# Kernel optimization log

Measured on AMD Instinct MI355X. Metric: run time of the kernel, lower is better.

The kernel has to match this reference:

```python
import jax, jax.numpy as jnp
import numpy as np

T, N, E = 64, 50000, 1600000
DYN, STAT, GH, RH = 1, 6, 32, 64


def setup_inputs() -> dict:
    key = jax.random.key(0)
    ks = jax.random.split(key, 12)
    s = 0.05
    return {
        "dyn_seq": jax.random.normal(ks[0], (T, N, DYN), jnp.float32),
        "static": jax.random.normal(ks[1], (N, STAT), jnp.float32),
        "edge_index": jax.random.randint(ks[2], (2, E), 0, N, jnp.int32),
        "gcn_w0": s * jax.random.normal(ks[3], (DYN + STAT, GH), jnp.float32),
        "gcn_b0": jnp.zeros((GH,), jnp.float32),
        "gcn_w1": s * jax.random.normal(ks[4], (GH, GH), jnp.float32),
        "gcn_b1": jnp.zeros((GH,), jnp.float32),
        "w_ih": s * jax.random.normal(ks[5], (3 * RH, GH), jnp.float32),
        "w_hh": s * jax.random.normal(ks[6], (3 * RH, RH), jnp.float32),
        "b_ih": jnp.zeros((3 * RH,), jnp.float32),
        "b_hh": jnp.zeros((3 * RH,), jnp.float32),
        "mlp_w1": s * jax.random.normal(ks[7], (RH, RH), jnp.float32),
        "mlp_b1": jnp.zeros((RH,), jnp.float32),
        "mlp_w2": s * jax.random.normal(ks[8], (1, RH), jnp.float32),
        "mlp_b2": jnp.zeros((1,), jnp.float32),
    }


def reference(dyn_seq, static, edge_index, gcn_w0, gcn_b0, gcn_w1, gcn_b1,
              w_ih, w_hh, b_ih, b_hh, mlp_w1, mlp_b1, mlp_w2, mlp_b2):
    n = static.shape[0]
    # GCNConv normalization (PyG default): add self-loops, sym norm D^-1/2 (A+I) D^-1/2
    loops = jnp.arange(n, dtype=edge_index.dtype)
    src = jnp.concatenate([edge_index[0], loops])
    dst = jnp.concatenate([edge_index[1], loops])
    deg = jax.ops.segment_sum(jnp.ones_like(dst, jnp.float32), dst, num_segments=n)
    dinv = jnp.where(deg > 0, jax.lax.rsqrt(deg), 0.0)
    norm = (dinv[src] * dinv[dst])[:, None]  # [E+N, 1]

    def gcn(h, w, b):
        h = h @ w  # transform first (small feature dim), then aggregate
        agg = jax.ops.segment_sum(h[src] * norm, dst, num_segments=n)
        return jax.nn.relu(agg + b)

    def step(x_t):  # x_t: [N, DYN]
        x = jnp.concatenate([x_t, static], axis=1)
        return gcn(gcn(x, gcn_w0, gcn_b0), gcn_w1, gcn_b1)

    H = jax.lax.map(step, dyn_seq)  # [T, N, GH] (sequential over T to bound memory)

    rh = w_hh.shape[1]

    def gru_step(h, x_t):  # torch nn.GRU cell math
        gx = x_t @ w_ih.T + b_ih
        gh = h @ w_hh.T + b_hh
        xr, xz, xn = jnp.split(gx, 3, axis=-1)
        hr, hz, hn = jnp.split(gh, 3, axis=-1)
        r = jax.nn.sigmoid(xr + hr)
        z = jax.nn.sigmoid(xz + hz)
        cand = jnp.tanh(xn + r * hn)
        h_new = (1.0 - z) * cand + z * h
        return h_new, None

    h0 = jnp.zeros((n, rh), H.dtype)
    h_last, _ = jax.lax.scan(gru_step, h0, H)  # last GRU output == out[:, -1, :]
    hid = jax.nn.relu(h_last @ mlp_w1.T + mlp_b1)
    return (hid @ mlp_w2.T + mlp_b2).squeeze(-1)  # [N]
```

## Files before the change

### kernel.cpp

```cpp
#include <hip/hip_runtime.h>
#include <hip/hip_bf16.h>

#define T_   64
#define N_   50000
#define E_   1600000
#define GH_  32
#define RH_  64
#define TB32_ 32
#define G32B_ 12500
#define GB_  782
#define NB_  196
#define AB_  12500

typedef _Float16 half_t;
typedef __attribute__((ext_vector_type(8))) _Float16 half8;
typedef __attribute__((ext_vector_type(4))) _Float16 half4;
typedef __attribute__((ext_vector_type(4))) float f32x4;
typedef __attribute__((ext_vector_type(4))) int i32x4;

static __device__ __forceinline__ float fast_sigmoid(float v) {
    float e = __expf(-v);
    return __builtin_amdgcn_rcpf(1.0f + e);
}
static __device__ __forceinline__ float fast_tanh(float v) {
    return 2.0f * fast_sigmoid(2.0f * v) - 1.0f;
}


__global__ __launch_bounds__(256)
void k_transpose(const float* __restrict__ dyn, half_t* __restrict__ dynT) {
    __shared__ float tile[64][65];
    int n0 = blockIdx.x * 64;
    int tx = threadIdx.x, ty = threadIdx.y;
#pragma unroll
    for (int r = 0; r < 16; ++r) {
        int t = r * 4 + ty;
        int n = n0 + tx;
        tile[t][tx] = (n < N_) ? dyn[(size_t)t * N_ + n] : 0.0f;
    }
    __syncthreads();
#pragma unroll
    for (int r = 0; r < 16; ++r) {
        int nl = r * 4 + ty;
        int n = n0 + nl;
        if (n < N_) dynT[(size_t)n * 64 + tx] = (half_t)tile[tx][nl];
    }
}

__global__ void k_hist(const int* __restrict__ src, const int* __restrict__ dst,
                       int* __restrict__ cnt) {
    int e = blockIdx.x * blockDim.x + threadIdx.x;
    if (e >= E_) return;
    atomicAdd(&cnt[dst[e] * 16 + (src[e] >> 12)], 1);
}

__global__ __launch_bounds__(256)
void k_scanA(const int* __restrict__ cnt, int* __restrict__ deg,
             int* __restrict__ row_ptr, int* __restrict__ bsum) {
    __shared__ int buf[256];
    int tid = threadIdx.x;
    int i = blockIdx.x * 256 + tid;
    int v = 0;
    if (i < N_) {
        const int4* c4 = (const int4*)(cnt + i * 16);
#pragma unroll
        for (int c = 0; c < 4; ++c) {
            int4 w = c4[c];
            v += w.x + w.y + w.z + w.w;
        }
        deg[i] = v;
    }
    buf[tid] = v;
    __syncthreads();
#pragma unroll
    for (int off = 1; off < 256; off <<= 1) {
        int t = (tid >= off) ? buf[tid - off] : 0;
        __syncthreads();
        buf[tid] += t;
        __syncthreads();
    }
    if (i < N_) row_ptr[i + 1] = buf[tid];
    if (tid == 255) bsum[blockIdx.x] = buf[255];
}
__global__ __launch_bounds__(256)
void k_scanB(int* __restrict__ bsum, int nb) {
    __shared__ int buf[256];
    int tid = threadIdx.x;
    buf[tid] = (tid < nb) ? bsum[tid] : 0;
    __syncthreads();
#pragma unroll
    for (int off = 1; off < 256; off <<= 1) {
        int t = (tid >= off) ? buf[tid - off] : 0;
        __syncthreads();
        buf[tid] += t;
        __syncthreads();
    }
    if (tid < nb) bsum[tid] = (tid > 0) ? buf[tid - 1] : 0;
}
__global__ __launch_bounds__(256)
void k_scanC(int* __restrict__ row_ptr, const int* __restrict__ bsum) {
    int i = blockIdx.x * 256 + threadIdx.x;
    if (i == 0) row_ptr[0] = 0;
    if (i < N_) row_ptr[i + 1] += bsum[blockIdx.x];
}

__global__ __launch_bounds__(256)
void k_rowscan(const int* __restrict__ row_ptr, int* __restrict__ cnt,
               int* __restrict__ rp2) {
    int n = blockIdx.x * 256 + threadIdx.x;
    if (n >= N_) return;
    int run = row_ptr[n];
#pragma unroll
    for (int t = 0; t < 16; ++t) {
        int c = cnt[n * 16 + t];
        rp2[n * 16 + t] = run;
        run += c;
        cnt[n * 16 + t] = 0;
    }
}

__global__ __launch_bounds__(256)
void k_node_init(const int* __restrict__ deg,
                 const float* __restrict__ statics,
                 const float* __restrict__ w0,
                 float* __restrict__ dinv,
                 float* __restrict__ selfn,
                 half_t* __restrict__ h0s) {
    int n = blockIdx.x * blockDim.x + threadIdx.x;
    if (n >= N_) return;
    float d  = (float)deg[n] + 1.0f;
    float di = rsqrtf(d);
    dinv[n] = di;
    selfn[n] = di * di;
    float s[6];
#pragma unroll
    for (int j = 0; j < 6; ++j) s[j] = statics[n * 6 + j];
    half8 o[4];
#pragma unroll
    for (int k = 0; k < GH_; ++k) {
        float v = 0.0f;
#pragma unroll
        for (int j = 0; j < 6; ++j) v += s[j] * w0[(1 + j) * GH_ + k];
        o[k >> 3][k & 7] = (half_t)v;
    }
    half8* dst8 = (half8*)(h0s + (size_t)n * GH_);
#pragma unroll
    for (int c = 0; c < 4; ++c) dst8[c] = o[c];
}

__global__ void k_scatter2(const int* __restrict__ src, const int* __restrict__ dst,
                           const float* __restrict__ dinv,
                           const int* __restrict__ rp2, int* __restrict__ cnt,
                           int2* __restrict__ erec) {
    int e = blockIdx.x * blockDim.x + threadIdx.x;
    if (e >= E_) return;
    int s = src[e], d = dst[e];
    int slot = d * 16 + (s >> 12);
    int pos = rp2[slot] + atomicAdd(&cnt[slot], 1);
    erec[pos] = make_int2(s, __float_as_int(dinv[s] * dinv[d]));
}

__global__ void k_wB(const float* __restrict__ wih, const float* __restrict__ whh,
                     half_t* __restrict__ wB) {
    int idx = blockIdx.x * 256 + threadIdx.x;
    if (idx >= 96 * 192) return;
    int j = idx & 7;
    int r = idx >> 3;
    int m = r & 15; r >>= 4;
    int q = r & 3;  r >>= 2;
    int nt = r % 12;
    int c = r / 12;
    int k = c * 32 + q * 8 + j;
    int col = nt * 16 + m;
    float v = (k < 32) ? wih[col * 32 + k] : whh[col * 64 + (k - 32)];
    wB[idx] = (half_t)v;
}

__global__ void k_w1B(const float* __restrict__ w1, half_t* __restrict__ w1B) {
    int idx = blockIdx.x * 256 + threadIdx.x;
    if (idx >= 1024) return;
    int j = idx & 7;
    int m = (idx >> 3) & 15;
    int q = (idx >> 7) & 3;
    int nt = idx >> 9;
    w1B[idx] = (half_t)w1[(q * 8 + j) * GH_ + nt * 16 + m];
}


static __device__ __forceinline__
void aall_body(int bid, const int* __restrict__ row_ptr, const int2* __restrict__ erec,
               const float* __restrict__ selfn, const half_t* __restrict__ dynT,
               half_t* __restrict__ aTh) {
    int wv = __builtin_amdgcn_readfirstlane(threadIdx.x >> 6);
    int n = bid * 4 + wv;
    int lane = threadIdx.x & 63;
    float acc = selfn[n] * (float)dynT[(size_t)n * 64 + lane];
    int e0 = row_ptr[n], e1 = row_ptr[n + 1];
    int e = e0;
    for (; e < e1 && (e & 3); ++e) {
        int2 r = erec[e];
        acc += __int_as_float(r.y) * (float)dynT[(size_t)r.x * 64 + lane];
    }
    for (; e + 4 <= e1; e += 4) {
        int4 p0 = *(const int4*)(erec + e);
        int4 p1 = *(const int4*)(erec + e + 2);
        float v0 = (float)dynT[(size_t)p0.x * 64 + lane];
        float v1 = (float)dynT[(size_t)p0.z * 64 + lane];
        float v2 = (float)dynT[(size_t)p1.x * 64 + lane];
        float v3 = (float)dynT[(size_t)p1.z * 64 + lane];
        acc += __int_as_float(p0.y) * v0 + __int_as_float(p0.w) * v1
             + __int_as_float(p1.y) * v2 + __int_as_float(p1.w) * v3;
    }
    for (; e < e1; ++e) {
        int2 r = erec[e];
        acc += __int_as_float(r.y) * (float)dynT[(size_t)r.x * 64 + lane];
    }
    aTh[(size_t)n * 64 + lane] = (half_t)acc;
}

static __device__ __forceinline__
void g16s_body(int bid, const int* __restrict__ row_ptr, const int2* __restrict__ erec,
               const float* __restrict__ selfn, const half_t* __restrict__ h0s,
               const float* __restrict__ b0, half_t* __restrict__ ch) {
    int gid = bid * 256 + threadIdx.x;
    int n = gid >> 2, q = gid & 3;
    if (n >= N_) return;
    const half8* f8 = (const half8*)h0s;
    float acc[8];
    {
        half8 sv = f8[(size_t)n * 4 + q];
        float sn = selfn[n];
#pragma unroll
        for (int i = 0; i < 8; ++i) acc[i] = sn * (float)sv[i];
    }
    int e0 = row_ptr[n], e1 = row_ptr[n + 1];
    int e = e0;
    for (; e < e1 && (e & 3); ++e) {
        int2 r = erec[e];
        float nm = __int_as_float(r.y);
        half8 v = f8[(size_t)r.x * 4 + q];
#pragma unroll
        for (int i = 0; i < 8; ++i) acc[i] += nm * (float)v[i];
    }
    for (; e + 4 <= e1; e += 4) {
        int4 p0 = *(const int4*)(erec + e);
        int4 p1 = *(const int4*)(erec + e + 2);
        half8 v0 = f8[(size_t)p0.x * 4 + q];
        half8 v1 = f8[(size_t)p0.z * 4 + q];
        half8 v2 = f8[(size_t)p1.x * 4 + q];
        half8 v3 = f8[(size_t)p1.z * 4 + q];
        float n0 = __int_as_float(p0.y), n1 = __int_as_float(p0.w);
        float n2 = __int_as_float(p1.y), n3 = __int_as_float(p1.w);
#pragma unroll
        for (int i = 0; i < 8; ++i)
            acc[i] += n0 * (float)v0[i] + n1 * (float)v1[i]
                    + n2 * (float)v2[i] + n3 * (float)v3[i];
    }
    for (; e < e1; ++e) {
        int2 r = erec[e];
        float nm = __int_as_float(r.y);
        half8 v = f8[(size_t)r.x * 4 + q];
#pragma unroll
        for (int i = 0; i < 8; ++i) acc[i] += nm * (float)v[i];
    }
    half8 o;
#pragma unroll
    for (int i = 0; i < 8; ++i) o[i] = (half_t)(acc[i] + b0[q * 8 + i]);
    *(half8*)(ch + (size_t)n * GH_ + q * 8) = o;
}

__global__ __launch_bounds__(256)
void k_aux(const int* __restrict__ row_ptr, const int2* __restrict__ erec,
           const float* __restrict__ selfn, const half_t* __restrict__ dynT,
           half_t* __restrict__ aTh, const half_t* __restrict__ h0s,
           const float* __restrict__ b0, half_t* __restrict__ ch) {
    if ((int)blockIdx.x < AB_)
        aall_body(blockIdx.x, row_ptr, erec, selfn, dynT, aTh);
    else
        g16s_body((int)blockIdx.x - AB_, row_ptr, erec, selfn, h0s, b0, ch);
}

__global__ __launch_bounds__(256)
void k_gather64(const int* __restrict__ row_ptr, const int2* __restrict__ erec,
                const float* __restrict__ selfn,
                const half_t* __restrict__ aTh,
                const half_t* __restrict__ ch,
                const float* __restrict__ w0,
                const half_t* __restrict__ w1B,
                const float* __restrict__ b1,
                half_t* __restrict__ xblk) {
    __shared__ half_t sh[4 * 64 * 40];
    int tid = threadIdx.x;
    int wv = __builtin_amdgcn_readfirstlane(tid >> 6);
    int n = blockIdx.x * 4 + wv;
    int l = tid & 63;
    int tg8 = (l >> 3) * 8;
    int kc = (l & 7) * 4;
    float w0r[4];
#pragma unroll
    for (int i = 0; i < 4; ++i) w0r[i] = w0[kc + i];

    const half_t* aBase = aTh + tg8;
    float acc[8][4];

    auto edge_acc = [&](half8 aa, half4 cc, float nmv) {
#pragma unroll
        for (int tt = 0; tt < 8; ++tt) {
#pragma unroll
            for (int i = 0; i < 4; ++i) {
                float hv = fmaxf(fmaf((float)aa[tt], w0r[i], (float)cc[i]), 0.0f);
                acc[tt][i] = fmaf(nmv, hv, acc[tt][i]);
            }
        }
    };

    {
        float sn = selfn[n];
        half8 a8 = *(const half8*)(aBase + (size_t)n * 64);
        half4 c4 = *(const half4*)(ch + (size_t)n * GH_ + kc);
#pragma unroll
        for (int tt = 0; tt < 8; ++tt) {
#pragma unroll
            for (int i = 0; i < 4; ++i) {
                float hv = fmaxf(fmaf((float)a8[tt], w0r[i], (float)c4[i]), 0.0f);
                acc[tt][i] = sn * hv;
            }
        }
    }

    int e0 = row_ptr[n], e1 = row_ptr[n + 1];
    int e = e0;
    if (e < e1 && (e & 1)) {
        int2 r = erec[e];
        half8 a8 = *(const half8*)(aBase + (size_t)r.x * 64);
        half4 c4 = *(const half4*)(ch + (size_t)r.x * GH_ + kc);
        edge_acc(a8, c4, __int_as_float(r.y));
        ++e;
    }
    for (; e + 2 <= e1; e += 2) {
        i32x4 p0 = *(const i32x4*)(erec + e);
        size_t s0 = (size_t)p0[0], s1 = (size_t)p0[2];
        half8 a80 = *(const half8*)(aBase + s0 * 64);
        half8 a81 = *(const half8*)(aBase + s1 * 64);
        half4 c40 = *(const half4*)(ch + s0 * GH_ + kc);
        half4 c41 = *(const half4*)(ch + s1 * GH_ + kc);
        edge_acc(a80, c40, __int_as_float(p0[1]));
        edge_acc(a81, c41, __int_as_float(p0[3]));
    }
    for (; e < e1; ++e) {
        int2 r = erec[e];
        half8 a8 = *(const half8*)(aBase + (size_t)r.x * 64);
        half4 c4 = *(const half4*)(ch + (size_t)r.x * GH_ + kc);
        edge_acc(a8, c4, __int_as_float(r.y));
    }

    half_t* shw = sh + wv * 64 * 40;
#pragma unroll
    for (int tt = 0; tt < 8; ++tt) {
        half4 o;
#pragma unroll
        for (int i = 0; i < 4; ++i) o[i] = (half_t)acc[tt][i];
        *(half4*)(shw + (tg8 + tt) * 40 + kc) = o;
    }

    int c16 = l & 15, q = l >> 4;
    const half8* wB8 = (const half8*)w1B;
    half8 bf0 = wB8[(0 * 4 + q) * 16 + c16];
    half8 bf1 = wB8[(1 * 4 + q) * 16 + c16];
    float b1v0 = b1[c16], b1v1 = b1[16 + c16];

    const f32x4 zero = {0.0f, 0.0f, 0.0f, 0.0f};
    half8 A[4];
#pragma unroll
    for (int b = 0; b < 4; ++b)
        A[b] = *(const half8*)(shw + (b * 16 + c16) * 40 + q * 8);
    f32x4 C0[4], C1[4];
#pragma unroll
    for (int b = 0; b < 4; ++b) {
        C0[b] = __builtin_amdgcn_mfma_f32_16x16x32_f16(A[b], bf0, zero, 0, 0, 0);
        C1[b] = __builtin_amdgcn_mfma_f32_16x16x32_f16(A[b], bf1, zero, 0, 0, 0);
    }
#pragma unroll
    for (int b = 0; b < 4; ++b)
#pragma unroll
        for (int reg = 0; reg < 4; ++reg) {
            int row = b * 16 + q * 4 + reg;
            shw[row * 40 + c16]      = (half_t)fmaxf(C0[b][reg] + b1v0, 0.0f);
            shw[row * 40 + 16 + c16] = (half_t)fmaxf(C1[b][reg] + b1v1, 0.0f);
        }

#pragma unroll
    for (int i = 0; i < 4; ++i) {
        int idx = i * 64 + l;
        int tl = idx >> 2;
        int kcol = (idx & 3) * 8;
        half8 v = *(const half8*)(shw + tl * 40 + kcol);
        *(half8*)(xblk + ((size_t)tl * N_ + n) * GH_ + kcol) = v;
    }
}

__global__ __launch_bounds__(256)
void k_gather32(const int* __restrict__ row_ptr, const int2* __restrict__ erec,
                const float* __restrict__ selfn,
                const half_t* __restrict__ aTh,
                const half_t* __restrict__ ch,
                const float* __restrict__ w0,
                const half_t* __restrict__ w1B,
                const float* __restrict__ b1,
                half_t* __restrict__ xblk,
                int h) {
    __shared__ half_t sh[4 * 32 * 40];
    int tid = threadIdx.x;
    int wv = __builtin_amdgcn_readfirstlane(tid >> 6);
    int n = blockIdx.x * 4 + wv;
    int l = tid & 63;
    int tg4 = (l >> 3) * 4;
    int kc = (l & 7) * 4;
    float w0r[4];
#pragma unroll
    for (int i = 0; i < 4; ++i) w0r[i] = w0[kc + i];
    const half_t* aBase = aTh + h * 32 + tg4;
    float acc[4][4];

    auto edge_acc = [&](half4 aa, half4 cc, float nmv) {
#pragma unroll
        for (int tt = 0; tt < 4; ++tt)
#pragma unroll
            for (int i = 0; i < 4; ++i) {
                float hv = fmaxf(fmaf((float)aa[tt], w0r[i], (float)cc[i]), 0.0f);
                acc[tt][i] = fmaf(nmv, hv, acc[tt][i]);
            }
    };

    {
        float sn = selfn[n];
        half4 a4 = *(const half4*)(aBase + (size_t)n * 64);
        half4 c4 = *(const half4*)(ch + (size_t)n * GH_ + kc);
#pragma unroll
        for (int tt = 0; tt < 4; ++tt)
#pragma unroll
            for (int i = 0; i < 4; ++i) {
                float hv = fmaxf(fmaf((float)a4[tt], w0r[i], (float)c4[i]), 0.0f);
                acc[tt][i] = sn * hv;
            }
    }

    int e0 = row_ptr[n], e1 = row_ptr[n + 1];
    int e = e0;
    if (e < e1 && (e & 1)) {
        int2 r = erec[e];
        half4 a4 = *(const half4*)(aBase + (size_t)r.x * 64);
        half4 c4 = *(const half4*)(ch + (size_t)r.x * GH_ + kc);
        edge_acc(a4, c4, __int_as_float(r.y));
        ++e;
    }
    for (; e + 4 <= e1; e += 4) {
        i32x4 p0 = *(const i32x4*)(erec + e);
        i32x4 p1 = *(const i32x4*)(erec + e + 2);
        size_t s0 = (size_t)p0[0], s1 = (size_t)p0[2];
        size_t s2 = (size_t)p1[0], s3 = (size_t)p1[2];
        half4 a40 = *(const half4*)(aBase + s0 * 64);
        half4 a41 = *(const half4*)(aBase + s1 * 64);
        half4 a42 = *(const half4*)(aBase + s2 * 64);
        half4 a43 = *(const half4*)(aBase + s3 * 64);
        half4 c40 = *(const half4*)(ch + s0 * GH_ + kc);
        half4 c41 = *(const half4*)(ch + s1 * GH_ + kc);
        half4 c42 = *(const half4*)(ch + s2 * GH_ + kc);
        half4 c43 = *(const half4*)(ch + s3 * GH_ + kc);
        edge_acc(a40, c40, __int_as_float(p0[1]));
        edge_acc(a41, c41, __int_as_float(p0[3]));
        edge_acc(a42, c42, __int_as_float(p1[1]));
        edge_acc(a43, c43, __int_as_float(p1[3]));
    }
    for (; e < e1; ++e) {
        int2 r = erec[e];
        half4 a4 = *(const half4*)(aBase + (size_t)r.x * 64);
        half4 c4 = *(const half4*)(ch + (size_t)r.x * GH_ + kc);
        edge_acc(a4, c4, __int_as_float(r.y));
    }

    half_t* shw = sh + wv * 32 * 40;
#pragma unroll
    for (int tt = 0; tt < 4; ++tt) {
        half4 o;
#pragma unroll
        for (int i = 0; i < 4; ++i) o[i] = (half_t)acc[tt][i];
        *(half4*)(shw + (tg4 + tt) * 40 + kc) = o;
    }

    int c16 = l & 15, q = l >> 4;
    const half8* wB8 = (const half8*)w1B;
    half8 bf0 = wB8[(0 * 4 + q) * 16 + c16];
    half8 bf1 = wB8[(1 * 4 + q) * 16 + c16];
    float b1v0 = b1[c16], b1v1 = b1[16 + c16];

    const f32x4 zero = {0.0f, 0.0f, 0.0f, 0.0f};
    half8 A0 = *(const half8*)(shw + (0 * 16 + c16) * 40 + q * 8);
    half8 A1 = *(const half8*)(shw + (1 * 16 + c16) * 40 + q * 8);
    f32x4 C00 = __builtin_amdgcn_mfma_f32_16x16x32_f16(A0, bf0, zero, 0, 0, 0);
    f32x4 C01 = __builtin_amdgcn_mfma_f32_16x16x32_f16(A0, bf1, zero, 0, 0, 0);
    f32x4 C10 = __builtin_amdgcn_mfma_f32_16x16x32_f16(A1, bf0, zero, 0, 0, 0);
    f32x4 C11 = __builtin_amdgcn_mfma_f32_16x16x32_f16(A1, bf1, zero, 0, 0, 0);
#pragma unroll
    for (int reg = 0; reg < 4; ++reg) {
        shw[(q * 4 + reg) * 40 + c16]           = (half_t)fmaxf(C00[reg] + b1v0, 0.0f);
        shw[(q * 4 + reg) * 40 + 16 + c16]      = (half_t)fmaxf(C01[reg] + b1v1, 0.0f);
        shw[(16 + q * 4 + reg) * 40 + c16]      = (half_t)fmaxf(C10[reg] + b1v0, 0.0f);
        shw[(16 + q * 4 + reg) * 40 + 16 + c16] = (half_t)fmaxf(C11[reg] + b1v1, 0.0f);
    }
#pragma unroll
    for (int i = 0; i < 2; ++i) {
        int idx = i * 64 + l;
        int tl = idx >> 2;
        int kcol = (idx & 3) * 8;
        half8 v = *(const half8*)(shw + tl * 40 + kcol);
        *(half8*)(xblk + ((size_t)tl * N_ + n) * GH_ + kcol) = v;
    }
}

#define HSTR_ 72
__global__ __launch_bounds__(256, 2)
void k_gru32(const half_t* __restrict__ xblk,
             const half_t* __restrict__ wB,
             const float* __restrict__ bih, const float* __restrict__ bhh,
             half_t* __restrict__ hA) {
    __shared__ half_t hL[64 * HSTR_];
    int tid = threadIdx.x;
    int nb0 = blockIdx.x * 64;
    for (int i = tid; i < 64 * 8; i += 256) {
        int node = i >> 3, ch = i & 7;
        half8 v = *(const half8*)(hA + (size_t)(nb0 + node) * RH_ + ch * 8);
        *(half8*)(hL + node * HSTR_ + ch * 8) = v;
    }
    __syncthreads();
    int lane = tid & 63;
    int wv = tid >> 6;
    int c16 = lane & 15, q = lane >> 4;
    const half8* wB8 = (const half8*)wB;
    half8 bfr[3][12];
#pragma unroll
    for (int c = 0; c < 3; ++c)
#pragma unroll
        for (int nt = 0; nt < 12; ++nt)
            bfr[c][nt] = wB8[((c * 12 + nt) * 4 + q) * 16 + c16];
    float br[4], bz[4], bnx[4], bnh[4];
#pragma unroll
    for (int jt = 0; jt < 4; ++jt) {
        int j = jt * 16 + c16;
        br[jt]  = bih[j] + bhh[j];
        bz[jt]  = bih[64 + j] + bhh[64 + j];
        bnx[jt] = bih[128 + j];
        bnh[jt] = bhh[128 + j];
    }
    int mrow = wv * 16 + c16;
    const half_t* hrow = hL + mrow * HSTR_;
    half_t hreg[4][4];
#pragma unroll
    for (int jt = 0; jt < 4; ++jt)
#pragma unroll
        for (int reg = 0; reg < 4; ++reg)
            hreg[jt][reg] = hL[(wv * 16 + q * 4 + reg) * HSTR_ + jt * 16 + c16];
    const f32x4 zero = {0.0f, 0.0f, 0.0f, 0.0f};
#pragma unroll 1
    for (int u = 0; u < TB32_; ++u) {
        half8 ax = __builtin_nontemporal_load(
            (const half8*)(xblk + ((size_t)u * N_ + nb0 + mrow) * GH_ + q * 8));
        half8 ah0 = *(const half8*)(hrow + q * 8);
        half8 ah1 = *(const half8*)(hrow + 32 + q * 8);
        f32x4 Crz[8], Cnx[4], Cnh[4];
#pragma unroll
        for (int nt = 0; nt < 8; ++nt) {
            Crz[nt] = __builtin_amdgcn_mfma_f32_16x16x32_f16(ax,  bfr[0][nt], zero,     0, 0, 0);
            Crz[nt] = __builtin_amdgcn_mfma_f32_16x16x32_f16(ah0, bfr[1][nt], Crz[nt], 0, 0, 0);
            Crz[nt] = __builtin_amdgcn_mfma_f32_16x16x32_f16(ah1, bfr[2][nt], Crz[nt], 0, 0, 0);
        }
#pragma unroll
        for (int nt = 0; nt < 4; ++nt) {
            Cnx[nt] = __builtin_amdgcn_mfma_f32_16x16x32_f16(ax,  bfr[0][8 + nt], zero,     0, 0, 0);
            Cnh[nt] = __builtin_amdgcn_mfma_f32_16x16x32_f16(ah0, bfr[1][8 + nt], zero,     0, 0, 0);
            Cnh[nt] = __builtin_amdgcn_mfma_f32_16x16x32_f16(ah1, bfr[2][8 + nt], Cnh[nt], 0, 0, 0);
        }
#pragma unroll
        for (int jt = 0; jt < 4; ++jt) {
#pragma unroll
            for (int reg = 0; reg < 4; ++reg) {
                int nl = wv * 16 + q * 4 + reg;
                int jj = jt * 16 + c16;
                float hold = (float)hreg[jt][reg];
                float r  = fast_sigmoid(Crz[jt][reg] + br[jt]);
                float z  = fast_sigmoid(Crz[4 + jt][reg] + bz[jt]);
                float cd = fast_tanh(Cnx[jt][reg] + bnx[jt] + r * (Cnh[jt][reg] + bnh[jt]));
                half_t hnew = (half_t)((1.0f - z) * cd + z * hold);
                hreg[jt][reg] = hnew;
                hL[nl * HSTR_ + jj] = hnew;
            }
        }
    }
    __syncthreads();
    for (int i = tid; i < 64 * 8; i += 256) {
        int node = i >> 3, ch = i & 7;
        half8 v = *(const half8*)(hL + node * HSTR_ + ch * 8);
        *(half8*)(hA + (size_t)(nb0 + node) * RH_ + ch * 8) = v;
    }
}

__global__ __launch_bounds__(256)
void k_mlp(const half_t* __restrict__ hA, const float* __restrict__ w1,
           const float* __restrict__ b1, const float* __restrict__ w2,
           const float* __restrict__ b2, float* __restrict__ out) {
    int n = blockIdx.x * blockDim.x + threadIdx.x;
    if (n >= N_) return;
    float h[RH_];
    const half8* h8 = (const half8*)(hA + (size_t)n * RH_);
#pragma unroll
    for (int c = 0; c < 8; ++c) {
        half8 v = h8[c];
#pragma unroll
        for (int i = 0; i < 8; ++i) h[c * 8 + i] = (float)v[i];
    }
    float acc = b2[0];
#pragma unroll 1
    for (int j = 0; j < RH_; ++j) {
        float v = b1[j];
#pragma unroll
        for (int k = 0; k < RH_; ++k) v += w1[j * RH_ + k] * h[k];
        v = v > 0.0f ? v : 0.0f;
        acc += w2[j] * v;
    }
    out[n] = acc;
}

extern "C" void kernel_launch(void* const* d_in, const int* in_sizes, int n_in,
                              void* d_out, int out_size, void* d_ws, size_t ws_size,
                              hipStream_t stream) {
    const float* dyn     = (const float*)d_in[0];
    const float* statics = (const float*)d_in[1];
    const int*   ei      = (const int*)d_in[2];
    const float* w0      = (const float*)d_in[3];
    const float* b0      = (const float*)d_in[4];
    const float* w1      = (const float*)d_in[5];
    const float* b1      = (const float*)d_in[6];
    const float* wih     = (const float*)d_in[7];
    const float* whh     = (const float*)d_in[8];
    const float* bih     = (const float*)d_in[9];
    const float* bhh     = (const float*)d_in[10];
    const float* mw1     = (const float*)d_in[11];
    const float* mb1     = (const float*)d_in[12];
    const float* mw2     = (const float*)d_in[13];
    const float* mb2     = (const float*)d_in[14];
    const int* src = ei;
    const int* dst = ei + E_;

    char* ws = (char*)d_ws;
    auto alloc = [&](size_t elems) {
        elems = (elems + 63) & ~(size_t)63;
        void* p = ws; ws += elems * 4; return p;
    };
    const int NPAD = N_ + 64;
    int*    deg     = (int*)alloc(N_);
    int*    row_ptr = (int*)alloc(N_ + 4);
    int*    bsum    = (int*)alloc(256);
    int*    cnt     = (int*)alloc((size_t)N_ * 16);
    int*    rp2     = (int*)alloc((size_t)N_ * 16);
    int2*   erec    = (int2*)alloc((size_t)E_ * 2);
    float*  dinv    = (float*)alloc(N_);
    float*  selfn   = (float*)alloc(N_);
    half_t* h0s     = (half_t*)alloc((size_t)N_ * GH_ / 2);
    half_t* ch      = (half_t*)alloc((size_t)N_ * GH_ / 2);
    half_t* aTh     = (half_t*)alloc((size_t)N_ * 64 / 2);
    half_t* hA      = (half_t*)alloc((size_t)NPAD * RH_ / 2);
    half_t* dynT    = (half_t*)alloc((size_t)N_ * 64 / 2);
    half_t* wB      = (half_t*)alloc(96 * 192 / 2);
    half_t* w1B     = (half_t*)alloc(1024 / 2);
    size_t used = (size_t)(ws - (char*)d_ws);
    size_t xblk64_bytes = ((size_t)64 * N_ + 64) * GH_ * sizeof(half_t);
    bool use64 = (ws_size >= used + xblk64_bytes + 4096);
    half_t* xblk = (half_t*)ws;

    auto cdiv = [](long long x, int b) { return (unsigned)((x + b - 1) / b); };
    const int B = 256;

    hipMemsetAsync(cnt, 0, (size_t)N_ * 16 * sizeof(int), stream);
    hipMemsetAsync(hA, 0, (size_t)NPAD * RH_ * sizeof(half_t), stream);

    k_transpose<<<cdiv(N_, 64), dim3(64, 4), 0, stream>>>(dyn, dynT);
    k_hist<<<cdiv(E_, B), B, 0, stream>>>(src, dst, cnt);
    k_scanA<<<NB_, B, 0, stream>>>(cnt, deg, row_ptr, bsum);
    k_scanB<<<1, B, 0, stream>>>(bsum, NB_);
    k_scanC<<<NB_, B, 0, stream>>>(row_ptr, bsum);
    k_rowscan<<<NB_, B, 0, stream>>>(row_ptr, cnt, rp2);
    k_node_init<<<NB_, B, 0, stream>>>(deg, statics, w0, dinv, selfn, h0s);
    k_scatter2<<<cdiv(E_, B), B, 0, stream>>>(src, dst, dinv, rp2, cnt, erec);
    k_wB<<<cdiv(96 * 192, B), B, 0, stream>>>(wih, whh, wB);
    k_w1B<<<4, B, 0, stream>>>(w1, w1B);
    k_aux<<<AB_ + GB_, B, 0, stream>>>(row_ptr, erec, selfn, dynT, aTh, h0s, b0, ch);

    if (use64) {
        k_gather64<<<G32B_, B, 0, stream>>>(row_ptr, erec, selfn, aTh, ch, w0,
                                            w1B, b1, xblk);
        k_gru32<<<GB_, B, 0, stream>>>(xblk, wB, bih, bhh, hA);
        k_gru32<<<GB_, B, 0, stream>>>(xblk + (size_t)32 * N_ * GH_, wB, bih, bhh, hA);
    } else {
        for (int h = 0; h < 2; ++h) {
            k_gather32<<<G32B_, B, 0, stream>>>(row_ptr, erec, selfn, aTh, ch, w0,
                                                w1B, b1, xblk, h);
            k_gru32<<<GB_, B, 0, stream>>>(xblk, wB, bih, bhh, hA);
        }
    }
    k_mlp<<<NB_, B, 0, stream>>>(hA, mw1, mb1, mw2, mb2, (float*)d_out);
}
```

Baseline: 939.2 us.

## Launch gather kernels with one wavefront per block and drop GRU register state

The two gather kernels now run one 64-lane block per node instead of four nodes per 256-thread block, so each block uses its own smaller shared buffer and finishes independently of its neighbours. Separately, the GRU kernel no longer keeps the previous hidden state in registers and rereads it from LDS at every timestep. The first change is meant to reduce tail imbalance from uneven node degrees, at the cost of four times as many blocks to schedule. The second lowers register pressure, possibly raising occupancy, but adds LDS reads inside the recurrent loop.

Result: faster. 914.6 us (-2.6%).

```diff
diff --git a/kernel.cpp b/kernel.cpp
--- a/kernel.cpp
+++ b/kernel.cpp
@@ -7,7 +7,6 @@
 #define GH_  32
 #define RH_  64
 #define TB32_ 32
-#define G32B_ 12500
 #define GB_  782
 #define NB_  196
 #define AB_  12500
@@ -280,7 +279,7 @@
         g16s_body((int)blockIdx.x - AB_, row_ptr, erec, selfn, h0s, b0, ch);
 }
 
-__global__ __launch_bounds__(256)
+__global__ __launch_bounds__(64)
 void k_gather64(const int* __restrict__ row_ptr, const int2* __restrict__ erec,
                 const float* __restrict__ selfn,
                 const half_t* __restrict__ aTh,
@@ -289,11 +288,9 @@
                 const half_t* __restrict__ w1B,
                 const float* __restrict__ b1,
                 half_t* __restrict__ xblk) {
-    __shared__ half_t sh[4 * 64 * 40];
-    int tid = threadIdx.x;
-    int wv = __builtin_amdgcn_readfirstlane(tid >> 6);
-    int n = blockIdx.x * 4 + wv;
-    int l = tid & 63;
+    __shared__ half_t shw[64 * 40];
+    int n = blockIdx.x;
+    int l = threadIdx.x;
     int tg8 = (l >> 3) * 8;
     int kc = (l & 7) * 4;
     float w0r[4];
@@ -354,7 +351,6 @@
         edge_acc(a8, c4, __int_as_float(r.y));
     }
 
-    half_t* shw = sh + wv * 64 * 40;
 #pragma unroll
     for (int tt = 0; tt < 8; ++tt) {
         half4 o;
@@ -399,7 +395,7 @@
     }
 }
 
-__global__ __launch_bounds__(256)
+__global__ __launch_bounds__(64)
 void k_gather32(const int* __restrict__ row_ptr, const int2* __restrict__ erec,
                 const float* __restrict__ selfn,
                 const half_t* __restrict__ aTh,
@@ -409,11 +405,9 @@
                 const float* __restrict__ b1,
                 half_t* __restrict__ xblk,
                 int h) {
-    __shared__ half_t sh[4 * 32 * 40];
-    int tid = threadIdx.x;
-    int wv = __builtin_amdgcn_readfirstlane(tid >> 6);
-    int n = blockIdx.x * 4 + wv;
-    int l = tid & 63;
+    __shared__ half_t shw[32 * 40];
+    int n = blockIdx.x;
+    int l = threadIdx.x;
     int tg4 = (l >> 3) * 4;
     int kc = (l & 7) * 4;
     float w0r[4];
@@ -479,7 +473,6 @@
         edge_acc(a4, c4, __int_as_float(r.y));
     }
 
-    half_t* shw = sh + wv * 32 * 40;
 #pragma unroll
     for (int tt = 0; tt < 4; ++tt) {
         half4 o;
@@ -554,12 +547,6 @@
     }
     int mrow = wv * 16 + c16;
     const half_t* hrow = hL + mrow * HSTR_;
-    half_t hreg[4][4];
-#pragma unroll
-    for (int jt = 0; jt < 4; ++jt)
-#pragma unroll
-        for (int reg = 0; reg < 4; ++reg)
-            hreg[jt][reg] = hL[(wv * 16 + q * 4 + reg) * HSTR_ + jt * 16 + c16];
     const f32x4 zero = {0.0f, 0.0f, 0.0f, 0.0f};
 #pragma unroll 1
     for (int u = 0; u < TB32_; ++u) {
@@ -586,13 +573,11 @@
             for (int reg = 0; reg < 4; ++reg) {
                 int nl = wv * 16 + q * 4 + reg;
                 int jj = jt * 16 + c16;
-                float hold = (float)hreg[jt][reg];
+                float hold = (float)hL[nl * HSTR_ + jj];
                 float r  = fast_sigmoid(Crz[jt][reg] + br[jt]);
                 float z  = fast_sigmoid(Crz[4 + jt][reg] + bz[jt]);
                 float cd = fast_tanh(Cnx[jt][reg] + bnx[jt] + r * (Cnh[jt][reg] + bnh[jt]));
-                half_t hnew = (half_t)((1.0f - z) * cd + z * hold);
-                hreg[jt][reg] = hnew;
-                hL[nl * HSTR_ + jj] = hnew;
+                hL[nl * HSTR_ + jj] = (half_t)((1.0f - z) * cd + z * hold);
             }
         }
     }
@@ -696,14 +681,14 @@
     k_aux<<<AB_ + GB_, B, 0, stream>>>(row_ptr, erec, selfn, dynT, aTh, h0s, b0, ch);
 
     if (use64) {
-        k_gather64<<<G32B_, B, 0, stream>>>(row_ptr, erec, selfn, aTh, ch, w0,
-                                            w1B, b1, xblk);
+        k_gather64<<<N_, 64, 0, stream>>>(row_ptr, erec, selfn, aTh, ch, w0,
+                                          w1B, b1, xblk);
         k_gru32<<<GB_, B, 0, stream>>>(xblk, wB, bih, bhh, hA);
         k_gru32<<<GB_, B, 0, stream>>>(xblk + (size_t)32 * N_ * GH_, wB, bih, bhh, hA);
     } else {
         for (int h = 0; h < 2; ++h) {
-            k_gather32<<<G32B_, B, 0, stream>>>(row_ptr, erec, selfn, aTh, ch, w0,
-                                                w1B, b1, xblk, h);
+            k_gather32<<<N_, 64, 0, stream>>>(row_ptr, erec, selfn, aTh, ch, w0,
+                                              w1B, b1, xblk, h);
             k_gru32<<<GB_, B, 0, stream>>>(xblk, wB, bih, bhh, hA);
         }
     }
```
